# Kernel optimization log

Hardware: AMD Instinct MI355X
Metric: run time of the kernel (lower is better)

## Reference

```python
import jax, jax.numpy as jnp
import numpy as np

EPS = 1e-12
B, S, H, NH = 4, 2048, 512, 8
DH = H // NH

def layernorm(x, g, b):
    mu = jnp.mean(x, axis=-1, keepdims=True)
    var = jnp.mean((x - mu) ** 2, axis=-1, keepdims=True)
    return (x - mu) * jax.lax.rsqrt(var + EPS) * g + b

def setup_inputs() -> dict:
    key = jax.random.key(0)
    ks = jax.random.split(key, 12)
    s = 0.02
    return {
        "hidden_states": jax.random.normal(ks[0], (B, S, H), dtype=jnp.float32),
        "attention_mask": jnp.zeros((B, 1, 1, S), dtype=jnp.float32),
        "ln1_g": jnp.ones((H,), jnp.float32), "ln1_b": jnp.zeros((H,), jnp.float32),
        "wq": jax.random.normal(ks[1], (H, H), jnp.float32) * s, "bq": jnp.zeros((H,), jnp.float32),
        "wk": jax.random.normal(ks[2], (H, H), jnp.float32) * s, "bk": jnp.zeros((H,), jnp.float32),
        "wv": jax.random.normal(ks[3], (H, H), jnp.float32) * s, "bv": jnp.zeros((H,), jnp.float32),
        "wo": jax.random.normal(ks[4], (H, H), jnp.float32) * s, "bo": jnp.zeros((H,), jnp.float32),
        "ln2_g": jnp.ones((H,), jnp.float32), "ln2_b": jnp.zeros((H,), jnp.float32),
    }

def _heads(x):  # [B,S,H] -> [B,NH,S,DH]
    return x.reshape(B, S, NH, DH).transpose(0, 2, 1, 3)

def reference(hidden_states, attention_mask, ln1_g, ln1_b, wq, bq, wk, bk, wv, bv, wo, bo, ln2_g, ln2_b):
    h = layernorm(hidden_states, ln1_g, ln1_b)  # Pre-LN
    q = _heads(h @ wq.T + bq)
    k = _heads(h @ wk.T + bk)
    v = _heads(h @ wv.T + bv)
    scores = jnp.einsum("bhqd,bhkd->bhqk", q, k) / jnp.sqrt(jnp.float32(DH))
    scores = scores + attention_mask  # additive BERT mask
    probs = jax.nn.softmax(scores, axis=-1)
    ctx = jnp.einsum("bhqk,bhkd->bhqd", probs, v)
    ctx = ctx.transpose(0, 2, 1, 3).reshape(B, S, H)
    # BertSelfOutput: LN(dense(ctx) + residual), residual is the LN'd hidden per module code
    out = layernorm(ctx @ wo.T + bo + h, ln2_g, ln2_b)
    return out
```

## Files before the change

kernel.cpp:

```cpp
#include <hip/hip_runtime.h>

typedef __bf16 bf16;
typedef __bf16 bf16x2 __attribute__((ext_vector_type(2)));
typedef __bf16 bf16x4 __attribute__((ext_vector_type(4)));
typedef __bf16 bf16x8 __attribute__((ext_vector_type(8)));
typedef float f32x4 __attribute__((ext_vector_type(4)));

typedef __attribute__((address_space(1))) const void g_void;
typedef __attribute__((address_space(3))) void l_void;

constexpr int Bsz = 4, S = 2048, H = 512, NH = 8, DH = 64;
constexpr int M = Bsz * S;
constexpr int K = H;
constexpr int WELEM = H * H;
constexpr float LOG2E  = 1.44269504f;
constexpr float QSCALE = 0.125f * LOG2E;

__global__ __launch_bounds__(256) void prep(
    const float* __restrict__ hidden, const float* __restrict__ ln1_g,
    const float* __restrict__ ln1_b,
    const float* __restrict__ w0, const float* __restrict__ w1,
    const float* __restrict__ w2, const float* __restrict__ w3,
    const float* __restrict__ mask,
    bf16* __restrict__ h, bf16* __restrict__ wb, float* __restrict__ mask2) {
    int bx = blockIdx.x;
    int t = threadIdx.x;
    if (bx < M) {
        int row = bx;
        float2 xv = *(const float2*)(hidden + (size_t)row * H + t * 2);
        float v0 = xv.x, v1 = xv.y;
        float s = v0 + v1, s2 = v0 * v0 + v1 * v1;
        for (int off = 1; off < 64; off <<= 1) {
            s  += __shfl_xor(s,  off, 64);
            s2 += __shfl_xor(s2, off, 64);
        }
        __shared__ float red[8];
        int wid = t >> 6;
        if ((t & 63) == 0) { red[wid * 2] = s; red[wid * 2 + 1] = s2; }
        __syncthreads();
        s  = red[0] + red[2] + red[4] + red[6];
        s2 = red[1] + red[3] + red[5] + red[7];
        float mu  = s * (1.0f / H);
        float var = s2 * (1.0f / H) - mu * mu;
        float inv = rsqrtf(var + 1e-12f);
        float2 gv = *(const float2*)(ln1_g + t * 2);
        float2 bv = *(const float2*)(ln1_b + t * 2);
        bf16x2 out;
        out.x = (bf16)((v0 - mu) * inv * gv.x + bv.x);
        out.y = (bf16)((v1 - mu) * inv * gv.y + bv.y);
        *(bf16x2*)(h + (size_t)row * H + t * 2) = out;
    } else if (bx < M + 1024) {
        int idx = bx - M;
        int y = idx >> 8, xx = idx & 255;
        const float* src = (y == 0) ? w0 : (y == 1) ? w1 : (y == 2) ? w2 : w3;
        bf16* d = wb + (size_t)y * WELEM;
        int i = (xx * 256 + t) * 4;
        float4 v = *(const float4*)(src + i);
        bf16x4 o;
        o.x = (bf16)v.x; o.y = (bf16)v.y; o.z = (bf16)v.z; o.w = (bf16)v.w;
        *(bf16x4*)(d + i) = o;
    } else {
        int i = (bx - M - 1024) * 256 + t;
        mask2[i] = mask[i] * LOG2E;
    }
}

__global__ __launch_bounds__(256) void ln_bf16_f32(
    const bf16* __restrict__ x, const float* __restrict__ g,
    const float* __restrict__ b, float* __restrict__ y) {
    int row = blockIdx.x;
    int t = threadIdx.x;
    bf16x2 xv = *(const bf16x2*)(x + (size_t)row * H + t * 2);
    float v0 = (float)xv.x, v1 = (float)xv.y;
    float s = v0 + v1, s2 = v0 * v0 + v1 * v1;
    for (int off = 1; off < 64; off <<= 1) {
        s  += __shfl_xor(s,  off, 64);
        s2 += __shfl_xor(s2, off, 64);
    }
    __shared__ float red[8];
    int wid = t >> 6;
    if ((t & 63) == 0) { red[wid * 2] = s; red[wid * 2 + 1] = s2; }
    __syncthreads();
    s  = red[0] + red[2] + red[4] + red[6];
    s2 = red[1] + red[3] + red[5] + red[7];
    float mu  = s * (1.0f / H);
    float var = s2 * (1.0f / H) - mu * mu;
    float inv = rsqrtf(var + 1e-12f);
    float2 gv = *(const float2*)(g + t * 2);
    float2 bv = *(const float2*)(b + t * 2);
    float2 out;
    out.x = (v0 - mu) * inv * gv.x + bv.x;
    out.y = (v1 - mu) * inv * gv.y + bv.y;
    *(float2*)(y + (size_t)row * H + t * 2) = out;
}

template<int BM, int BN, int MI, int NI>
__device__ inline void gemm_mainloop512(const bf16* __restrict__ A,
                                        const bf16* __restrict__ W,
                                        int bm, int bn,
                                        bf16* As, bf16* Bs, f32x4 acc[MI][NI]) {
    int t = threadIdx.x;
    int lane = t & 63, wid = t >> 6;
    int quad = lane >> 4, n = lane & 15;
    int wm = wid & 1, wn = wid >> 1;
    int sw = (n & 7) * 8;
    int srow = lane >> 3;
    int scol = (lane & 7) * 8;
    constexpr int APW = BM / 64;
    constexpr int BPW = BN / 64;
    constexpr int RM = MI * 16;
    constexpr int RN = NI * 16;
    for (int kt = 0; kt < K; kt += 64) {
        __syncthreads();
        #pragma unroll
        for (int i = 0; i < APW; i++) {
            int chunk = wid * APW + i;
            int row = chunk * 8 + srow;
            int csrc = scol ^ ((row & 7) * 8);
            __builtin_amdgcn_global_load_lds(
                (g_void*)&A[(size_t)(bm + row) * K + kt + csrc],
                (l_void*)&As[chunk * 512], 16, 0, 0);
        }
        #pragma unroll
        for (int i = 0; i < BPW; i++) {
            int chunk = wid * BPW + i;
            int row = chunk * 8 + srow;
            int csrc = scol ^ ((row & 7) * 8);
            __builtin_amdgcn_global_load_lds(
                (g_void*)&W[(size_t)(bn + row) * K + kt + csrc],
                (l_void*)&Bs[chunk * 512], 16, 0, 0);
        }
        __syncthreads();
        #pragma unroll
        for (int half = 0; half < 2; half++) {
            bf16x8 af[MI], bfr[NI];
            int c = (half * 32 + quad * 8) ^ sw;
            #pragma unroll
            for (int mi = 0; mi < MI; mi++)
                af[mi] = *(const bf16x8*)&As[(wm * RM + mi * 16 + n) * 64 + c];
            #pragma unroll
            for (int ni = 0; ni < NI; ni++)
                bfr[ni] = *(const bf16x8*)&Bs[(wn * RN + ni * 16 + n) * 64 + c];
            #pragma unroll
            for (int mi = 0; mi < MI; mi++)
                #pragma unroll
                for (int ni = 0; ni < NI; ni++)
                    acc[mi][ni] = __builtin_amdgcn_mfma_f32_16x16x32_bf16(
                        af[mi], bfr[ni], acc[mi][ni], 0, 0, 0);
        }
    }
}

__global__ __launch_bounds__(512, 4) void gemm_qkv(
    const bf16* __restrict__ h, const bf16* __restrict__ wb,
    const float* __restrict__ bq, const float* __restrict__ bk,
    const float* __restrict__ bv,
    bf16* __restrict__ qd, bf16* __restrict__ kd, bf16* __restrict__ vtd) {
    __shared__ alignas(16) bf16 smem[17408];
    bf16* As = smem;
    bf16* Bs = smem + 8192;
    int bm = blockIdx.x * 128, bn = blockIdx.y * 128, z = blockIdx.z;
    const bf16* W = wb + (size_t)z * WELEM;
    const float* bias = (z == 0) ? bq : (z == 1) ? bk : bv;
    f32x4 acc[4][2];
    for (int mi = 0; mi < 4; mi++)
        for (int ni = 0; ni < 2; ni++)
            for (int r = 0; r < 4; r++) acc[mi][ni][r] = 0.0f;
    gemm_mainloop512<128, 128, 4, 2>(h, W, bm, bn, As, Bs, acc);
    int t = threadIdx.x;
    int lane = t & 63, wid = t >> 6;
    int quad = lane >> 4, n = lane & 15;
    int wm = wid & 1, wn = wid >> 1;
    if (z < 2) {
        bf16* dst = (z == 0) ? qd : kd;
        for (int mi = 0; mi < 4; mi++)
            for (int ni = 0; ni < 2; ni++)
                for (int r = 0; r < 4; r++) {
                    int i = bm + wm * 64 + mi * 16 + quad * 4 + r;
                    int j = bn + wn * 32 + ni * 16 + n;
                    float val = acc[mi][ni][r] + bias[j];
                    if (z == 0) val *= QSCALE;
                    int b = i >> 11, srow = i & (S - 1);
                    int nh = j >> 6, d = j & (DH - 1);
                    dst[(((size_t)(b * NH + nh)) * S + srow) * DH + d] = (bf16)val;
                }
    } else {
        __syncthreads();
        bf16* T = smem;
        for (int mi = 0; mi < 4; mi++)
            for (int ni = 0; ni < 2; ni++)
                for (int r = 0; r < 4; r++) {
                    int il = wm * 64 + mi * 16 + quad * 4 + r;
                    int jl = wn * 32 + ni * 16 + n;
                    float val = acc[mi][ni][r] + bias[bn + jl];
                    T[jl * 136 + il] = (bf16)val;
                }
        __syncthreads();
        int b = bm >> 11, srow0 = bm & (S - 1);
        int c16 = t & 15;
        #pragma unroll
        for (int p = 0; p < 4; p++) {
            int jl = (t >> 4) + p * 32;
            int j = bn + jl;
            int nh = j >> 6, d = j & (DH - 1);
            bf16x8 v = *(const bf16x8*)&T[jl * 136 + c16 * 8];
            *(bf16x8*)&vtd[(((size_t)(b * NH + nh)) * DH + d) * S
                           + srow0 + c16 * 8] = v;
        }
    }
}

__global__ __launch_bounds__(512, 4) void gemm_out(
    const bf16* __restrict__ ctx, const bf16* __restrict__ wo,
    const float* __restrict__ bo, const bf16* __restrict__ resid,
    bf16* __restrict__ dst) {
    __shared__ alignas(16) bf16 As[64 * 64];
    __shared__ alignas(16) bf16 Bs[128 * 64];
    int bm = blockIdx.x * 64, bn = blockIdx.y * 128;
    f32x4 acc[2][2];
    for (int mi = 0; mi < 2; mi++)
        for (int ni = 0; ni < 2; ni++)
            for (int r = 0; r < 4; r++) acc[mi][ni][r] = 0.0f;
    gemm_mainloop512<64, 128, 2, 2>(ctx, wo, bm, bn, As, Bs, acc);
    int lane = threadIdx.x & 63, wid = threadIdx.x >> 6;
    int quad = lane >> 4, n = lane & 15;
    int wm = wid & 1, wn = wid >> 1;
    for (int mi = 0; mi < 2; mi++)
        for (int ni = 0; ni < 2; ni++)
            for (int r = 0; r < 4; r++) {
                int i = bm + wm * 32 + mi * 16 + quad * 4 + r;
                int j = bn + wn * 32 + ni * 16 + n;
                float val = acc[mi][ni][r] + bo[j]
                          + (float)resid[(size_t)i * H + j];
                dst[(size_t)i * H + j] = (bf16)val;
            }
}

constexpr int LDP9 = 72;

#if __has_builtin(__builtin_amdgcn_exp2f)
#define EXP2(x) __builtin_amdgcn_exp2f(x)
#else
#define EXP2(x) exp2f(x)
#endif

__global__ __launch_bounds__(512, 4) void attn_kernel(
    const bf16* __restrict__ q, const bf16* __restrict__ k,
    const bf16* __restrict__ vt, const float* __restrict__ mask2,
    bf16* __restrict__ ctx) {
    int bh = blockIdx.y;
    int b = bh >> 3, nh = bh & 7;
    int t = threadIdx.x, wid = t >> 6, lane = t & 63;
    int quad = lane >> 4, n = lane & 15;
    int qg = wid >> 1, kh = wid & 1;
    int qbase = blockIdx.x * 128 + qg * 32;
    int kO = kh * 64;

    const bf16* Qp = q  + (size_t)bh * S * DH;
    const bf16* Kp = k  + (size_t)bh * S * DH;
    const bf16* Vt = vt + (size_t)bh * DH * S;
    const float* mrow = mask2 + (size_t)b * S;

    __shared__ alignas(16) bf16 smem[34816];
    bf16* Ks = smem;
    bf16* Vs = smem + 8192;
    bf16* Pw = smem + 16384 + wid * (32 * LDP9);

    int sw = (n & 7) * 8;

    int krow = t >> 3;
    int kcs  = ((t & 7) * 8) ^ ((krow & 7) * 8);
    size_t koff = (size_t)krow * DH + kcs;
    int vr0 = t >> 4,        vc0 = ((t & 15) * 8) ^ ((vr0 & 7) * 8);
    int vr1 = (t + 512) >> 4, vc1 = ((t & 15) * 8) ^ ((vr1 & 7) * 8);
    size_t voff0 = (size_t)vr0 * S + vc0;
    size_t voff1 = (size_t)vr1 * S + vc1;

    bf16x8 qf[2][2];
    #pragma unroll
    for (int qt = 0; qt < 2; qt++)
        #pragma unroll
        for (int hh = 0; hh < 2; hh++)
            qf[qt][hh] = *(const bf16x8*)
                &Qp[(size_t)(qbase + qt * 16 + n) * DH + hh * 32 + quad * 8];

    f32x4 O[2][4];
    #pragma unroll
    for (int qt = 0; qt < 2; qt++)
        for (int i = 0; i < 4; i++)
            for (int r = 0; r < 4; r++) O[qt][i][r] = 0.0f;
    float l_run[2] = {0.0f, 0.0f};

    uint4 kreg  = *(const uint4*)&Kp[koff];
    uint4 vreg0 = *(const uint4*)&Vt[voff0];
    uint4 vreg1 = *(const uint4*)&Vt[voff1];

    for (int kb = 0; kb < S; kb += 128) {
        __syncthreads();
        *(uint4*)&Ks[(size_t)t * 8] = kreg;
        *(uint4*)&Vs[(size_t)t * 8] = vreg0;
        *(uint4*)&Vs[(size_t)(t + 512) * 8] = vreg1;
        __syncthreads();

        if (kb + 128 < S) {
            kreg  = *(const uint4*)&Kp[koff + (size_t)(kb + 128) * DH];
            vreg0 = *(const uint4*)&Vt[voff0 + (kb + 128)];
            vreg1 = *(const uint4*)&Vt[voff1 + (kb + 128)];
        }

        #pragma unroll
        for (int kt = 0; kt < 4; kt++) {
            const bf16* kr = &Ks[(kO + kt * 16 + n) * 64];
            bf16x8 ka = *(const bf16x8*)&kr[(quad * 8) ^ sw];
            bf16x8 kc = *(const bf16x8*)&kr[(32 + quad * 8) ^ sw];
            float4 mk = *(const float4*)&mrow[kb + kO + kt * 16 + quad * 4];
            #pragma unroll
            for (int qt = 0; qt < 2; qt++) {
                f32x4 s;
                for (int r = 0; r < 4; r++) s[r] = 0.0f;
                s = __builtin_amdgcn_mfma_f32_16x16x32_bf16(ka, qf[qt][0], s, 0, 0, 0);
                s = __builtin_amdgcn_mfma_f32_16x16x32_bf16(kc, qf[qt][1], s, 0, 0, 0);
                float p0 = EXP2(s[0] + mk.x);
                float p1 = EXP2(s[1] + mk.y);
                float p2 = EXP2(s[2] + mk.z);
                float p3 = EXP2(s[3] + mk.w);
                l_run[qt] += (p0 + p1) + (p2 + p3);
                bf16x4 w;
                w[0] = (bf16)p0; w[1] = (bf16)p1; w[2] = (bf16)p2; w[3] = (bf16)p3;
                *(bf16x4*)&Pw[(qt * 16 + n) * LDP9 + kt * 16 + quad * 4] = w;
            }
        }

        __builtin_amdgcn_s_setprio(1);
        #pragma unroll
        for (int ks = 0; ks < 2; ks++)
            #pragma unroll
            for (int qt = 0; qt < 2; qt++) {
                bf16x8 pf = *(const bf16x8*)
                    &Pw[(qt * 16 + n) * LDP9 + ks * 32 + quad * 8];
                #pragma unroll
                for (int dt = 0; dt < 4; dt++) {
                    bf16x8 vf = *(const bf16x8*)
                        &Vs[(dt * 16 + n) * 128 + ((kO + ks * 32 + quad * 8) ^ sw)];
                    O[qt][dt] = __builtin_amdgcn_mfma_f32_16x16x32_bf16(
                        vf, pf, O[qt][dt], 0, 0, 0);
                }
            }
        __builtin_amdgcn_s_setprio(0);
    }

    float* Ob = (float*)smem;
    float* Lb = Ob + 4 * 32 * 68;
    __syncthreads();
    if (kh) {
        #pragma unroll
        for (int qt = 0; qt < 2; qt++) {
            #pragma unroll
            for (int dt = 0; dt < 4; dt++)
                *(f32x4*)&Ob[(qg * 32 + qt * 16 + n) * 68 + dt * 16 + quad * 4]
                    = O[qt][dt];
            Lb[(qg * 2 + qt) * 64 + lane] = l_run[qt];
        }
    }
    __syncthreads();
    if (!kh) {
        #pragma unroll
        for (int qt = 0; qt < 2; qt++) {
            float l = l_run[qt] + Lb[(qg * 2 + qt) * 64 + lane];
            l += __shfl_xor(l, 16, 64);
            l += __shfl_xor(l, 32, 64);
            float linv = 1.0f / l;
            int srow = qbase + qt * 16 + n;
            #pragma unroll
            for (int dt = 0; dt < 4; dt++) {
                f32x4 po = *(const f32x4*)
                    &Ob[(qg * 32 + qt * 16 + n) * 68 + dt * 16 + quad * 4];
                bf16x4 o4;
                for (int r = 0; r < 4; r++)
                    o4[r] = (bf16)((O[qt][dt][r] + po[r]) * linv);
                int col = nh * 64 + dt * 16 + quad * 4;
                *(bf16x4*)&ctx[((size_t)(b * S + srow)) * H + col] = o4;
            }
        }
    }
}

extern "C" void kernel_launch(void* const* d_in, const int* in_sizes, int n_in,
                              void* d_out, int out_size, void* d_ws, size_t ws_size,
                              hipStream_t stream) {
    const float* hidden = (const float*)d_in[0];
    const float* mask   = (const float*)d_in[1];
    const float* ln1_g  = (const float*)d_in[2];
    const float* ln1_b  = (const float*)d_in[3];
    const float* wq = (const float*)d_in[4],  *bq = (const float*)d_in[5];
    const float* wk = (const float*)d_in[6],  *bk = (const float*)d_in[7];
    const float* wv = (const float*)d_in[8],  *bv = (const float*)d_in[9];
    const float* wo = (const float*)d_in[10], *bo = (const float*)d_in[11];
    const float* ln2_g = (const float*)d_in[12];
    const float* ln2_b = (const float*)d_in[13];

    const size_t T = (size_t)M * H;
    bf16* wb  = (bf16*)d_ws;
    bf16* h   = wb  + (size_t)4 * WELEM;
    bf16* qd  = h   + T;
    bf16* kd  = qd  + T;
    bf16* vtd = kd  + T;
    bf16* ctx = vtd + T;
    float* mask2 = (float*)(ctx + T);
    bf16* tmp = qd;

    prep<<<M + 1024 + 32, 256, 0, stream>>>(
        hidden, ln1_g, ln1_b, wq, wk, wv, wo, mask, h, wb, mask2);
    gemm_qkv<<<dim3(M / 128, H / 128, 3), 512, 0, stream>>>(
        h, wb, bq, bk, bv, qd, kd, vtd);
    attn_kernel<<<dim3(S / 128, Bsz * NH), 512, 0, stream>>>(qd, kd, vtd, mask2, ctx);
    gemm_out<<<dim3(M / 64, H / 128), 512, 0, stream>>>(
        ctx, wb + (size_t)3 * WELEM, bo, h, tmp);
    ln_bf16_f32<<<M, 256, 0, stream>>>(tmp, ln2_g, ln2_b, (float*)d_out);
}
```

Measured before the change: 183.1 us.

## Load K and V fragments directly from global memory in attention

Drops the shared-memory staging of K and V tiles, along with its register prefetch and the two block barriers per iteration. Each wave now reads its MFMA K and V fragments straight from global memory and relies on L1/L2 caching, which shrinks LDS use and may raise occupancy. In exchange, the two warps sharing a key half reload the same data, accesses are less coalesced, and there is no explicit prefetch to hide global latency.

```diff
diff --git a/kernel.cpp b/kernel.cpp
--- a/kernel.cpp
+++ b/kernel.cpp
@@ -261,20 +261,8 @@
     const bf16* Vt = vt + (size_t)bh * DH * S;
     const float* mrow = mask2 + (size_t)b * S;
 
-    __shared__ alignas(16) bf16 smem[34816];
-    bf16* Ks = smem;
-    bf16* Vs = smem + 8192;
-    bf16* Pw = smem + 16384 + wid * (32 * LDP9);
-
-    int sw = (n & 7) * 8;
-
-    int krow = t >> 3;
-    int kcs  = ((t & 7) * 8) ^ ((krow & 7) * 8);
-    size_t koff = (size_t)krow * DH + kcs;
-    int vr0 = t >> 4,        vc0 = ((t & 15) * 8) ^ ((vr0 & 7) * 8);
-    int vr1 = (t + 512) >> 4, vc1 = ((t & 15) * 8) ^ ((vr1 & 7) * 8);
-    size_t voff0 = (size_t)vr0 * S + vc0;
-    size_t voff1 = (size_t)vr1 * S + vc1;
+    __shared__ alignas(16) bf16 smem[18432];
+    bf16* Pw = smem + wid * (32 * LDP9);
 
     bf16x8 qf[2][2];
     #pragma unroll
@@ -291,28 +279,12 @@
             for (int r = 0; r < 4; r++) O[qt][i][r] = 0.0f;
     float l_run[2] = {0.0f, 0.0f};
 
-    uint4 kreg  = *(const uint4*)&Kp[koff];
-    uint4 vreg0 = *(const uint4*)&Vt[voff0];
-    uint4 vreg1 = *(const uint4*)&Vt[voff1];
-
     for (int kb = 0; kb < S; kb += 128) {
-        __syncthreads();
-        *(uint4*)&Ks[(size_t)t * 8] = kreg;
-        *(uint4*)&Vs[(size_t)t * 8] = vreg0;
-        *(uint4*)&Vs[(size_t)(t + 512) * 8] = vreg1;
-        __syncthreads();
-
-        if (kb + 128 < S) {
-            kreg  = *(const uint4*)&Kp[koff + (size_t)(kb + 128) * DH];
-            vreg0 = *(const uint4*)&Vt[voff0 + (kb + 128)];
-            vreg1 = *(const uint4*)&Vt[voff1 + (kb + 128)];
-        }
-
         #pragma unroll
         for (int kt = 0; kt < 4; kt++) {
-            const bf16* kr = &Ks[(kO + kt * 16 + n) * 64];
-            bf16x8 ka = *(const bf16x8*)&kr[(quad * 8) ^ sw];
-            bf16x8 kc = *(const bf16x8*)&kr[(32 + quad * 8) ^ sw];
+            const bf16* krg = &Kp[(size_t)(kb + kO + kt * 16 + n) * DH];
+            bf16x8 ka = *(const bf16x8*)&krg[quad * 8];
+            bf16x8 kc = *(const bf16x8*)&krg[32 + quad * 8];
             float4 mk = *(const float4*)&mrow[kb + kO + kt * 16 + quad * 4];
             #pragma unroll
             for (int qt = 0; qt < 2; qt++) {
@@ -341,7 +313,8 @@
                 #pragma unroll
                 for (int dt = 0; dt < 4; dt++) {
                     bf16x8 vf = *(const bf16x8*)
-                        &Vs[(dt * 16 + n) * 128 + ((kO + ks * 32 + quad * 8) ^ sw)];
+                        &Vt[(size_t)(dt * 16 + n) * S
+                            + kb + kO + ks * 32 + quad * 8];
                     O[qt][dt] = __builtin_amdgcn_mfma_f32_16x16x32_bf16(
                         vf, pf, O[qt][dt], 0, 0, 0);
                 }
```

After: 254.3 us. 1.39x slower.

## Fuse output projection GEMM with second LayerNorm into one kernel

Applied to the files above, without the earlier changes.

Replaces the separate output-projection GEMM and bf16 LayerNorm kernel with one kernel. Each block now computes a full 32x512 row tile, adds bias and residual, stages the fp32 results in shared memory and applies LayerNorm in place. This removes one launch and the bf16 round trip of the intermediate through global memory, and keeps the pre-LN values in fp32. In exchange every block reloads the whole Wo weight for each K tile, uses about 68KB of shared memory, has no double buffering, and the grid shrinks to 256 blocks.

```diff
diff --git a/kernel.cpp b/kernel.cpp
--- a/kernel.cpp
+++ b/kernel.cpp
@@ -63,35 +63,6 @@
         int i = (bx - M - 1024) * 256 + t;
         mask2[i] = mask[i] * LOG2E;
     }
-}
-
-__global__ __launch_bounds__(256) void ln_bf16_f32(
-    const bf16* __restrict__ x, const float* __restrict__ g,
-    const float* __restrict__ b, float* __restrict__ y) {
-    int row = blockIdx.x;
-    int t = threadIdx.x;
-    bf16x2 xv = *(const bf16x2*)(x + (size_t)row * H + t * 2);
-    float v0 = (float)xv.x, v1 = (float)xv.y;
-    float s = v0 + v1, s2 = v0 * v0 + v1 * v1;
-    for (int off = 1; off < 64; off <<= 1) {
-        s  += __shfl_xor(s,  off, 64);
-        s2 += __shfl_xor(s2, off, 64);
-    }
-    __shared__ float red[8];
-    int wid = t >> 6;
-    if ((t & 63) == 0) { red[wid * 2] = s; red[wid * 2 + 1] = s2; }
-    __syncthreads();
-    s  = red[0] + red[2] + red[4] + red[6];
-    s2 = red[1] + red[3] + red[5] + red[7];
-    float mu  = s * (1.0f / H);
-    float var = s2 * (1.0f / H) - mu * mu;
-    float inv = rsqrtf(var + 1e-12f);
-    float2 gv = *(const float2*)(g + t * 2);
-    float2 bv = *(const float2*)(b + t * 2);
-    float2 out;
-    out.x = (v0 - mu) * inv * gv.x + bv.x;
-    out.y = (v1 - mu) * inv * gv.y + bv.y;
-    *(float2*)(y + (size_t)row * H + t * 2) = out;
 }
 
 template<int BM, int BN, int MI, int NI>
@@ -210,30 +181,94 @@
     }
 }
 
-__global__ __launch_bounds__(512, 4) void gemm_out(
+__global__ __launch_bounds__(512, 4) void gemm_out_ln2(
     const bf16* __restrict__ ctx, const bf16* __restrict__ wo,
     const float* __restrict__ bo, const bf16* __restrict__ resid,
-    bf16* __restrict__ dst) {
-    __shared__ alignas(16) bf16 As[64 * 64];
-    __shared__ alignas(16) bf16 Bs[128 * 64];
-    int bm = blockIdx.x * 64, bn = blockIdx.y * 128;
-    f32x4 acc[2][2];
-    for (int mi = 0; mi < 2; mi++)
-        for (int ni = 0; ni < 2; ni++)
-            for (int r = 0; r < 4; r++) acc[mi][ni][r] = 0.0f;
-    gemm_mainloop512<64, 128, 2, 2>(ctx, wo, bm, bn, As, Bs, acc);
-    int lane = threadIdx.x & 63, wid = threadIdx.x >> 6;
+    const float* __restrict__ g2, const float* __restrict__ b2,
+    float* __restrict__ out) {
+    __shared__ alignas(16) bf16 smem[34816];
+    bf16* As = smem;
+    bf16* Bs = smem + 2048;
+    int bm = blockIdx.x * 32;
+    int t = threadIdx.x;
+    int lane = t & 63, wid = t >> 6;
     int quad = lane >> 4, n = lane & 15;
     int wm = wid & 1, wn = wid >> 1;
-    for (int mi = 0; mi < 2; mi++)
-        for (int ni = 0; ni < 2; ni++)
-            for (int r = 0; r < 4; r++) {
-                int i = bm + wm * 32 + mi * 16 + quad * 4 + r;
-                int j = bn + wn * 32 + ni * 16 + n;
-                float val = acc[mi][ni][r] + bo[j]
-                          + (float)resid[(size_t)i * H + j];
-                dst[(size_t)i * H + j] = (bf16)val;
-            }
+    int sw = (n & 7) * 8;
+    int srow = lane >> 3;
+    int scol = (lane & 7) * 8;
+    f32x4 acc[8];
+    #pragma unroll
+    for (int ni = 0; ni < 8; ni++)
+        for (int r = 0; r < 4; r++) acc[ni][r] = 0.0f;
+    for (int kt = 0; kt < K; kt += 64) {
+        __syncthreads();
+        if (wid < 4) {
+            int chunk = wid;
+            int row = chunk * 8 + srow;
+            int csrc = scol ^ ((row & 7) * 8);
+            __builtin_amdgcn_global_load_lds(
+                (g_void*)&ctx[(size_t)(bm + row) * K + kt + csrc],
+                (l_void*)&As[chunk * 512], 16, 0, 0);
+        }
+        #pragma unroll
+        for (int i = 0; i < 8; i++) {
+            int chunk = wid * 8 + i;
+            int row = chunk * 8 + srow;
+            int csrc = scol ^ ((row & 7) * 8);
+            __builtin_amdgcn_global_load_lds(
+                (g_void*)&wo[(size_t)row * K + kt + csrc],
+                (l_void*)&Bs[chunk * 512], 16, 0, 0);
+        }
+        __syncthreads();
+        #pragma unroll
+        for (int half = 0; half < 2; half++) {
+            int c = (half * 32 + quad * 8) ^ sw;
+            bf16x8 af = *(const bf16x8*)&As[(wm * 16 + n) * 64 + c];
+            bf16x8 bfr[8];
+            #pragma unroll
+            for (int ni = 0; ni < 8; ni++)
+                bfr[ni] = *(const bf16x8*)&Bs[(wn * 128 + ni * 16 + n) * 64 + c];
+            #pragma unroll
+            for (int ni = 0; ni < 8; ni++)
+                acc[ni] = __builtin_amdgcn_mfma_f32_16x16x32_bf16(
+                    af, bfr[ni], acc[ni], 0, 0, 0);
+        }
+    }
+    __syncthreads();
+    float* Cf = (float*)smem;
+    #pragma unroll
+    for (int ni = 0; ni < 8; ni++)
+        #pragma unroll
+        for (int r = 0; r < 4; r++) {
+            int il = wm * 16 + quad * 4 + r;
+            int j = wn * 128 + ni * 16 + n;
+            float val = acc[ni][r] + bo[j]
+                      + (float)resid[(size_t)(bm + il) * H + j];
+            Cf[il * 516 + j] = val;
+        }
+    __syncthreads();
+    int row = t >> 4, l16 = t & 15;
+    float s = 0.0f, s2 = 0.0f;
+    #pragma unroll
+    for (int c = 0; c < 32; c++) {
+        float v = Cf[row * 516 + l16 + 16 * c];
+        s += v; s2 += v * v;
+    }
+    s  += __shfl_xor(s, 1, 64);  s2 += __shfl_xor(s2, 1, 64);
+    s  += __shfl_xor(s, 2, 64);  s2 += __shfl_xor(s2, 2, 64);
+    s  += __shfl_xor(s, 4, 64);  s2 += __shfl_xor(s2, 4, 64);
+    s  += __shfl_xor(s, 8, 64);  s2 += __shfl_xor(s2, 8, 64);
+    float mu  = s * (1.0f / H);
+    float var = s2 * (1.0f / H) - mu * mu;
+    float inv = rsqrtf(var + 1e-12f);
+    float* orow = out + (size_t)(bm + row) * H;
+    #pragma unroll
+    for (int c = 0; c < 32; c++) {
+        int col = l16 + 16 * c;
+        float v = Cf[row * 516 + col];
+        orow[col] = (v - mu) * inv * g2[col] + b2[col];
+    }
 }
 
 constexpr int LDP9 = 72;
@@ -407,14 +442,12 @@
     bf16* vtd = kd  + T;
     bf16* ctx = vtd + T;
     float* mask2 = (float*)(ctx + T);
-    bf16* tmp = qd;
 
     prep<<<M + 1024 + 32, 256, 0, stream>>>(
         hidden, ln1_g, ln1_b, wq, wk, wv, wo, mask, h, wb, mask2);
     gemm_qkv<<<dim3(M / 128, H / 128, 3), 512, 0, stream>>>(
         h, wb, bq, bk, bv, qd, kd, vtd);
     attn_kernel<<<dim3(S / 128, Bsz * NH), 512, 0, stream>>>(qd, kd, vtd, mask2, ctx);
-    gemm_out<<<dim3(M / 64, H / 128), 512, 0, stream>>>(
-        ctx, wb + (size_t)3 * WELEM, bo, h, tmp);
-    ln_bf16_f32<<<M, 256, 0, stream>>>(tmp, ln2_g, ln2_b, (float*)d_out);
-}
+    gemm_out_ln2<<<M / 32, 512, 0, stream>>>(
+        ctx, wb + (size_t)3 * WELEM, bo, h, ln2_g, ln2_b, (float*)d_out);
+}
```

After: 190.1 us. +3.8%, slower.
